# Kernel optimization log

Measured on AMD Instinct MI355X. Metric: run time of the kernel, lower is better.

Reference implementation:

```python
import jax, jax.numpy as jnp
import numpy as np

ENERGY = 0.4  # target low-frequency energy ratio (ctor default energy=0.4)


def setup_inputs() -> dict:
    key = jax.random.key(0)
    x = jax.random.normal(key, (8, 64, 256, 256), dtype=jnp.float32)
    return {"x": x}


def _min_cutoff_map(H, W):
    """For each pixel of the fftshifted spectrum, the smallest cutoff c such that
    the pixel lies inside the central box [crow-c:crow+c, ccol-c:ccol+c].
    A pixel (r, cc) is inside iff c >= max(-dr, dr+1) and c >= max(-dc, dc+1)."""
    crow, ccol = H // 2, W // 2
    dr = np.arange(H) - crow
    dc = np.arange(W) - ccol
    mr = np.maximum(-dr, dr + 1)
    mc = np.maximum(-dc, dc + 1)
    return np.maximum(mr[:, None], mc[None, :]).astype(np.int32)  # [H, W]


def reference(x):
    B, C, H, W = x.shape
    # fp32 FFT (matches the autocast-disabled fft in the original)
    fshift = jnp.fft.fftshift(jnp.fft.fft2(x.astype(jnp.float32)), axes=(-2, -1))

    minc = jnp.asarray(_min_cutoff_map(H, W))          # [H, W] int32
    nseg = max(H // 2, W // 2) + 1                      # static
    K = min(H, W) // 2                                  # candidates are 1..K-1

    # Radial (box) cumulative energy profile of channel 0, one pass per sample.
    mag2 = jnp.abs(fshift[:, 0]) ** 2                   # [B, H, W]
    ids = minc.reshape(-1)
    per_box = jax.vmap(
        lambda m: jax.ops.segment_sum(m.reshape(-1), ids, num_segments=nseg)
    )(mag2)                                             # [B, nseg]
    cum = jnp.cumsum(per_box, axis=-1)                  # cum[b, c] = box-energy at cutoff c
    total = cum[:, -1]
    target = ENERGY * total

    found = cum[:, 1:K] >= target[:, None]              # candidates c = 1..K-1
    first = jnp.argmax(found, axis=-1) + 1              # smallest satisfying c
    cutoff = jnp.where(jnp.any(found, axis=-1), first, 5)  # fallback 5, as in torch

    # Zero the central box per sample (broadcast over channels), then inverse FFT.
    keep = (minc[None, None, :, :] > cutoff[:, None, None, None]).astype(jnp.float32)
    hp = fshift * keep
    out = jnp.abs(jnp.fft.ifft2(jnp.fft.ifftshift(hp, axes=(-2, -1))))
    return out
```

## Files before the change

kernel.cpp:

```cpp
#include <hip/hip_runtime.h>
#include <hip/hip_fp16.h>
#include <math.h>

#define RESERVE 16384

__device__ __forceinline__ float2 cadd(float2 a, float2 b){ return make_float2(a.x+b.x, a.y+b.y); }
__device__ __forceinline__ float2 csub(float2 a, float2 b){ return make_float2(a.x-b.x, a.y-b.y); }
__device__ __forceinline__ float2 cmul(float2 a, float2 b){ return make_float2(a.x*b.x - a.y*b.y, a.x*b.y + a.y*b.x); }
__device__ __forceinline__ float2 cmulc(float2 a, float2 b){
  return make_float2(a.x*b.x + a.y*b.y, a.x*b.y - a.y*b.x); }
__device__ __forceinline__ __half2 f2h(float2 v){ return __floats2half2_rn(v.x, v.y); }
__device__ __forceinline__ float2 h2f(__half2 h){ return __half22float2(h); }

#define SCHED_FENCE() __builtin_amdgcn_sched_barrier(0x7F)

__device__ __forceinline__ constexpr int rho4(int r) { return ((r & 3) << 2) | (r >> 2); }

template<int DIR> __device__ __forceinline__ float2 twc(float2 z, float c, float s) {
  const float si = (DIR < 0) ? s : -s;
  return make_float2(c*z.x - si*z.y, c*z.y + si*z.x);
}
template<int DIR> __device__ __forceinline__ float2 mulmi(float2 z) {
  return (DIR < 0) ? make_float2(z.y, -z.x) : make_float2(-z.y, z.x);
}

template<int DIR, bool REV>
__device__ __forceinline__ void fft16(float2* v) {
  #define IX(i) (REV ? rho4(i) : (i))
  #pragma unroll
  for (int j0 = 0; j0 < 4; ++j0) {
    float2 a0 = v[IX(j0)], a1 = v[IX(j0+4)], a2 = v[IX(j0+8)], a3 = v[IX(j0+12)];
    float2 t0 = cadd(a0,a2), t1 = csub(a0,a2), t2 = cadd(a1,a3), d = csub(a1,a3);
    float2 t3 = (DIR < 0) ? make_float2(d.y,-d.x) : make_float2(-d.y,d.x);
    v[IX(j0)]    = cadd(t0,t2);
    v[IX(j0+4)]  = cadd(t1,t3);
    v[IX(j0+8)]  = csub(t0,t2);
    v[IX(j0+12)] = csub(t1,t3);
  }
  v[IX(5)]  = twc<DIR>(v[IX(5)],  0.92387953f, -0.38268343f);
  v[IX(6)]  = twc<DIR>(v[IX(6)],  0.70710678f, -0.70710678f);
  v[IX(7)]  = twc<DIR>(v[IX(7)],  0.38268343f, -0.92387953f);
  v[IX(9)]  = twc<DIR>(v[IX(9)],  0.70710678f, -0.70710678f);
  v[IX(10)] = mulmi<DIR>(v[IX(10)]);
  v[IX(11)] = twc<DIR>(v[IX(11)], -0.70710678f, -0.70710678f);
  v[IX(13)] = twc<DIR>(v[IX(13)],  0.38268343f, -0.92387953f);
  v[IX(14)] = twc<DIR>(v[IX(14)], -0.70710678f, -0.70710678f);
  v[IX(15)] = twc<DIR>(v[IX(15)], -0.92387953f,  0.38268343f);
  #pragma unroll
  for (int k1 = 0; k1 < 4; ++k1) {
    float2 a0 = v[IX(4*k1)], a1 = v[IX(4*k1+1)], a2 = v[IX(4*k1+2)], a3 = v[IX(4*k1+3)];
    float2 t0 = cadd(a0,a2), t1 = csub(a0,a2), t2 = cadd(a1,a3), d = csub(a1,a3);
    float2 t3 = (DIR < 0) ? make_float2(d.y,-d.x) : make_float2(-d.y,d.x);
    v[IX(4*k1)]   = cadd(t0,t2);
    v[IX(4*k1+1)] = cadd(t1,t3);
    v[IX(4*k1+2)] = csub(t0,t2);
    v[IX(4*k1+3)] = csub(t1,t3);
  }
  #undef IX
}

__device__ __forceinline__ void make_twf(int l, float2* twf) {
  float s, c;
  sincospif((float)l * (-1.0f/128.0f), &s, &c);
  const float2 w = make_float2(c, s);
  twf[0] = make_float2(1.f, 0.f);
  #pragma unroll
  for (int k = 1; k < 16; ++k) twf[k] = cmul(twf[k-1], w);
}

template<int DIR, bool REV1, bool HB>
__device__ __forceinline__ void fft256g(float2* v, void* trb, int l, const float2* twf) {
  fft16<DIR, REV1>(v);
  if (HB) {
    __half2* t = (__half2*)trb;
    #pragma unroll
    for (int r = 0; r < 16; ++r) {
      const int k1 = REV1 ? r : rho4(r);
      float2 z = v[r];
      z = (DIR < 0) ? cmul(twf[k1], z) : cmulc(twf[k1], z);
      t[k1 * 17 + l] = f2h(z);
    }
    SCHED_FENCE();
    #pragma unroll
    for (int j = 0; j < 16; ++j) v[j] = h2f(t[l * 17 + j]);
  } else {
    float2* t = (float2*)trb;
    #pragma unroll
    for (int r = 0; r < 16; ++r) {
      const int k1 = REV1 ? r : rho4(r);
      float2 z = v[r];
      z = (DIR < 0) ? cmul(twf[k1], z) : cmulc(twf[k1], z);
      t[k1 * 17 + l] = z;
    }
    SCHED_FENCE();
    #pragma unroll
    for (int j = 0; j < 16; ++j) v[j] = ((float2*)trb)[l * 17 + j];
  }
  SCHED_FENCE();
  fft16<DIR, false>(v);
}

#define GS32 276
#define GS16 280

__device__ __forceinline__ int SW(int row, int col) {
  return (row << 8) + (col ^ ((row & 7) << 2) ^ ((row & 1) << 4));
}
__device__ __forceinline__ int SW16(int r, int ul) {
  return (r << 4) + (ul ^ (r & 14));
}


__global__ __launch_bounds__(256) void k_pass1(const float* __restrict__ x,
    __half2* __restrict__ Bt, int img0, int istep) {
  __shared__ __align__(16) char smraw[16384];
  __shared__ __align__(16) float2 trbf[16 * GS32];
  float*   rowstage = (float*)smraw;
  __half2* outtile  = (__half2*)smraw;
  const int tid = threadIdx.x, g = tid >> 4, l = tid & 15;
  const int slot = blockIdx.y, img = img0 + slot * istep;
  const int r0 = blockIdx.x << 4;
  float2 twf[16]; make_twf(l, twf);
  const float* xsrc = x + ((size_t)img << 16) + (r0 << 8);
  #pragma unroll
  for (int it = 0; it < 4; ++it) {
    const int L = it * 1024 + tid * 4;
    const float4 d = *reinterpret_cast<const float4*>(xsrc + L);
    *reinterpret_cast<float4*>(rowstage + SW(L >> 8, L & 255)) = d;
  }
  __syncthreads();
  float2 v[16];
  #pragma unroll
  for (int j = 0; j < 16; ++j)
    v[j] = make_float2(rowstage[SW(g, l + (j << 4))], 0.f);
  __syncthreads();
  fft256g<-1, false, false>(v, trbf + g * GS32, l, twf);
  #pragma unroll
  for (int rr = 0; rr < 16; ++rr)
    outtile[SW(g, l + (rho4(rr) << 4))] = f2h(v[rr]);
  __syncthreads();
  __half2* bdst = Bt + ((size_t)slot << 16) + (r0 << 4);
  #pragma unroll
  for (int it = 0; it < 4; ++it) {
    const int L = it * 1024 + tid * 4;
    const int p = L >> 8, rl = (L >> 4) & 15, ul0 = L & 15;
    const int4 d = *reinterpret_cast<const int4*>(outtile + SW(rl, (p << 4) + ul0));
    *reinterpret_cast<int4*>(bdst + (p << 12) + (L & 255)) = d;
  }
}

__global__ __launch_bounds__(256) void k_pass2(const __half2* __restrict__ Bt,
    __half2* __restrict__ Ct, const int* __restrict__ cutoffs, int img0, int istep) {
  __shared__ __align__(16) char smraw[16384];
  __shared__ __align__(16) __half2 trbh[16 * GS16];
  __half2* instage = (__half2*)smraw;
  __half2* outtile = (__half2*)smraw;
  const int tid = threadIdx.x, g = tid >> 4, l = tid & 15;
  const int slot = blockIdx.y, img = img0 + slot * istep;
  const int p = blockIdx.x;
  const int cut = cutoffs[img >> 6];
  float2 twf[16]; make_twf(l, twf);
  const __half2* bsrc = Bt + ((size_t)slot << 16) + (p << 12);
  #pragma unroll
  for (int it = 0; it < 4; ++it) {
    const int L = it * 1024 + tid * 4;
    const int4 d = *reinterpret_cast<const int4*>(bsrc + L);
    const int r = L >> 4, ul0 = L & 15;
    const int i0 = SW16(r, ul0);
    *reinterpret_cast<int2*>(instage + i0) = make_int2(d.x, d.y);
    *reinterpret_cast<int2*>(instage + (i0 ^ 2)) = make_int2(d.z, d.w);
  }
  __syncthreads();
  __half2 hv[16];
  #pragma unroll
  for (int j = 0; j < 16; ++j) hv[j] = instage[SW16(l + (j << 4), g)];
  __syncthreads();
  const int u = (p << 4) + g;
  float2 v[16];
  #pragma unroll
  for (int j = 0; j < 16; ++j) v[j] = h2f(hv[j]);
  fft256g<-1, false, true>(v, trbh + g * GS16, l, twf);
  if ((u < cut) | (u >= 256 - cut)) {
    #pragma unroll
    for (int rr = 0; rr < 16; ++rr) {
      const int vi = l + (rho4(rr) << 4);
      if (vi < cut || vi >= 256 - cut) v[rr] = make_float2(0.f, 0.f);
    }
  }
  fft256g<1, true, true>(v, trbh + g * GS16, l, twf);
  #pragma unroll
  for (int rr = 0; rr < 16; ++rr)
    outtile[SW16(l + (rho4(rr) << 4), g)] = f2h(v[rr]);
  __syncthreads();
  __half2* cdst = Ct + ((size_t)slot << 16) + (p << 12);
  #pragma unroll
  for (int it = 0; it < 4; ++it) {
    const int L = it * 1024 + tid * 4;
    const int r = L >> 4, ul0 = L & 15;
    const int i0 = SW16(r, ul0);
    const int2 a = *reinterpret_cast<const int2*>(outtile + i0);
    const int2 b = *reinterpret_cast<const int2*>(outtile + (i0 ^ 2));
    *reinterpret_cast<int4*>(cdst + L) = make_int4(a.x, a.y, b.x, b.y);
  }
}

__global__ __launch_bounds__(256) void k_pass3(const __half2* __restrict__ Ct,
    float* __restrict__ out, int img0, int istep) {
  __shared__ __align__(16) char smraw[16384];
  __shared__ __align__(16) __half2 trbh[16 * GS16];
  __half2* instage  = (__half2*)smraw;
  float*   outstage = (float*)smraw;
  const int tid = threadIdx.x, g = tid >> 4, l = tid & 15;
  const int slot = blockIdx.y, img = img0 + slot * istep;
  const int r0 = blockIdx.x << 4;
  float2 twf[16]; make_twf(l, twf);
  #pragma unroll
  for (int k = 0; k < 16; ++k) { twf[k].x *= 0.0625f; twf[k].y *= 0.0625f; }
  const __half2* csrc = Ct + ((size_t)slot << 16) + (r0 << 4);
  #pragma unroll
  for (int it = 0; it < 4; ++it) {
    const int L = it * 1024 + tid * 4;
    const int p = L >> 8, rl = (L >> 4) & 15, ul0 = L & 15;
    const int4 d = *reinterpret_cast<const int4*>(csrc + (p << 12) + (L & 255));
    *reinterpret_cast<int4*>(instage + SW(rl, (p << 4) + ul0)) = d;
  }
  __syncthreads();
  __half2 hv[16];
  #pragma unroll
  for (int j = 0; j < 16; ++j) hv[j] = instage[SW(g, l + (j << 4))];
  __syncthreads();
  float2 v[16];
  #pragma unroll
  for (int j = 0; j < 16; ++j) v[j] = h2f(hv[j]);
  fft256g<1, false, true>(v, trbh + g * GS16, l, twf);
  #pragma unroll
  for (int rr = 0; rr < 16; ++rr) {
    const float2 z = v[rr];
    outstage[SW(g, l + (rho4(rr) << 4))] =
        __builtin_amdgcn_sqrtf(z.x*z.x + z.y*z.y) * (1.f/4096.f);
  }
  __syncthreads();
  float* odst = out + ((size_t)img << 16) + (r0 << 8);
  #pragma unroll
  for (int it = 0; it < 4; ++it) {
    const int L = it * 1024 + tid * 4;
    const float4 d = *reinterpret_cast<const float4*>(outstage + SW(L >> 8, L & 255));
    *reinterpret_cast<float4*>(odst + L) = d;
  }
}

__global__ __launch_bounds__(256) void k_hist(const __half2* __restrict__ Bt,
    double* __restrict__ bins, int slot0, int sstep, int batch0) {
  __shared__ __align__(16) __half2 instage[4096];
  __shared__ __align__(16) float2 trbf[16 * GS32];
  __shared__ float whist[4][132];
  const int tid = threadIdx.x, g = tid >> 4, l = tid & 15, wave = tid >> 6;
  const int lb = blockIdx.y;
  const int batch = batch0 + lb;
  const size_t slot = (size_t)(slot0 + lb * sstep);
  const int p = blockIdx.x;
  const int u = (p << 4) + g;
  float2 twf[16]; make_twf(l, twf);
  for (int i = tid & 63; i < 132; i += 64) whist[wave][i] = 0.f;
  const __half2* bsrc = Bt + (slot << 16) + (p << 12);
  #pragma unroll
  for (int it = 0; it < 4; ++it) {
    const int L = it * 1024 + tid * 4;
    const int4 d = *reinterpret_cast<const int4*>(bsrc + L);
    const int r = L >> 4, ul0 = L & 15;
    const int i0 = SW16(r, ul0);
    *reinterpret_cast<int2*>(instage + i0) = make_int2(d.x, d.y);
    *reinterpret_cast<int2*>(instage + (i0 ^ 2)) = make_int2(d.z, d.w);
  }
  __syncthreads();
  float2 v[16];
  #pragma unroll
  for (int j = 0; j < 16; ++j) v[j] = h2f(instage[SW16(l + (j << 4), g)]);
  fft256g<-1, false, false>(v, trbf + g * GS32, l, twf);
  const int fc = (u < 128) ? u + 1 : 256 - u;
  #pragma unroll
  for (int rr = 0; rr < 16; ++rr) {
    const int vi = l + (rho4(rr) << 4);
    const int fu = (vi < 128) ? vi + 1 : 256 - vi;
    const int seg = fu > fc ? fu : fc;
    const float2 z = v[rr];
    atomicAdd(&whist[wave][seg], z.x*z.x + z.y*z.y);
  }
  __syncthreads();
  for (int s = tid; s < 129; s += 256) {
    const float sum = whist[0][s] + whist[1][s] + whist[2][s] + whist[3][s];
    if (sum != 0.f) atomicAdd(&bins[batch * 129 + s], (double)sum);
  }
}

__global__ void k_cutoff(const double* __restrict__ bins, int* __restrict__ cutoffs) {
  const int b = threadIdx.x;
  if (b < 8) {
    const double* Bv = bins + b * 129;
    double total = 0.0;
    for (int s = 0; s < 129; ++s) total += Bv[s];
    const double target = 0.4 * total;
    double cum = Bv[0];
    int cut = 5;
    bool found = false;
    for (int s = 1; s <= 127; ++s) {
      cum += Bv[s];
      if (!found && cum >= target) { cut = s; found = true; }
    }
    cutoffs[b] = cut;
  }
}

extern "C" void kernel_launch(void* const* d_in, const int* in_sizes, int n_in,
                              void* d_out, int out_size, void* d_ws, size_t ws_size,
                              hipStream_t stream) {
  const float* x = (const float*)d_in[0];
  float* out = (float*)d_out;
  char* wsb = (char*)d_ws;
  double* bins    = (double*)wsb;
  int*    cutoffs = (int*)(wsb + 8448);
  char*   payload = wsb + RESERVE;

  size_t avail = (ws_size > RESERVE) ? ws_size - (size_t)RESERVE : 0;
  long long Gl = (long long)(avail / 524288);
  int G = (Gl > 512) ? 512 : (int)Gl;
  if (G < 1) G = 1;
  __half2* Bt = (__half2*)payload;
  __half2* Ct = (__half2*)(payload + (size_t)G * 262144);

  hipMemsetAsync(bins, 0, 8 * 129 * sizeof(double), stream);
  dim3 blk(256, 1, 1);

  if (G >= 512) {
    k_pass1<<<dim3(16, 512), blk, 0, stream>>>(x, Bt, 0, 1);
    k_hist <<<dim3(16, 8),   blk, 0, stream>>>(Bt, bins, 0, 64, 0);
    k_cutoff<<<dim3(1), dim3(64), 0, stream>>>(bins, cutoffs);
    k_pass2<<<dim3(16, 512), blk, 0, stream>>>(Bt, Ct, cutoffs, 0, 1);
    k_pass3<<<dim3(16, 512), blk, 0, stream>>>(Ct, out, 0, 1);
  } else {
    int Gp = G > 8 ? 8 : G;
    for (int b0 = 0; b0 < 8; b0 += Gp) {
      int n = (8 - b0 < Gp) ? (8 - b0) : Gp;
      k_pass1<<<dim3(16, n), blk, 0, stream>>>(x, Bt, b0 * 64, 64);
      k_hist <<<dim3(16, n), blk, 0, stream>>>(Bt, bins, 0, 1, b0);
    }
    k_cutoff<<<dim3(1), dim3(64), 0, stream>>>(bins, cutoffs);
    for (int g0 = 0; g0 < 512; g0 += G) {
      int n = (512 - g0 < G) ? (512 - g0) : G;
      k_pass1<<<dim3(16, n), blk, 0, stream>>>(x, Bt, g0, 1);
      k_pass2<<<dim3(16, n), blk, 0, stream>>>(Bt, Ct, cutoffs, g0, 1);
      k_pass3<<<dim3(16, n), blk, 0, stream>>>(Ct, out, g0, 1);
    }
  }
}
```

Baseline: 209.8 us.

## Skip identity column FFTs outside cutoff band and alias shared buffers

Pass2 blocks whose column group lies entirely outside the zeroed low-frequency band now exit early, because the forward and inverse column FFT would be an identity. Pass3 reads those columns directly from the row-FFT buffer, scaled by 256 to undo the missing normalization. Shared staging and transpose buffers are merged into one aliased region, with extra barriers, to reduce LDS use and allow more resident blocks. The fp16 rescale could lose precision or overflow, and how much work is skipped depends on the data-dependent cutoff.

```diff
diff --git a/kernel.cpp b/kernel.cpp
--- a/kernel.cpp
+++ b/kernel.cpp
@@ -113,10 +113,10 @@
 
 __global__ __launch_bounds__(256) void k_pass1(const float* __restrict__ x,
     __half2* __restrict__ Bt, int img0, int istep) {
-  __shared__ __align__(16) char smraw[16384];
-  __shared__ __align__(16) float2 trbf[16 * GS32];
+  __shared__ __align__(16) char smraw[16 * GS32 * 8];
   float*   rowstage = (float*)smraw;
   __half2* outtile  = (__half2*)smraw;
+  float2*  trbf     = (float2*)smraw;
   const int tid = threadIdx.x, g = tid >> 4, l = tid & 15;
   const int slot = blockIdx.y, img = img0 + slot * istep;
   const int r0 = blockIdx.x << 4;
@@ -135,6 +135,7 @@
     v[j] = make_float2(rowstage[SW(g, l + (j << 4))], 0.f);
   __syncthreads();
   fft256g<-1, false, false>(v, trbf + g * GS32, l, twf);
+  __syncthreads();
   #pragma unroll
   for (int rr = 0; rr < 16; ++rr)
     outtile[SW(g, l + (rho4(rr) << 4))] = f2h(v[rr]);
@@ -151,16 +152,19 @@
 
 __global__ __launch_bounds__(256) void k_pass2(const __half2* __restrict__ Bt,
     __half2* __restrict__ Ct, const int* __restrict__ cutoffs, int img0, int istep) {
-  __shared__ __align__(16) char smraw[16384];
-  __shared__ __align__(16) __half2 trbh[16 * GS16];
+  __shared__ __align__(16) char smraw[16 * GS16 * 4];
   __half2* instage = (__half2*)smraw;
   __half2* outtile = (__half2*)smraw;
+  __half2* trbh    = (__half2*)smraw;
   const int tid = threadIdx.x, g = tid >> 4, l = tid & 15;
   const int slot = blockIdx.y, img = img0 + slot * istep;
   const int p = blockIdx.x;
   const int cut = cutoffs[img >> 6];
+  const bool kept = (p * 16 >= cut) && (p * 16 + 15 < 256 - cut);
+  if (kept) return;
+  const __half2* bsrc = Bt + ((size_t)slot << 16) + (p << 12);
+  __half2* cdst = Ct + ((size_t)slot << 16) + (p << 12);
   float2 twf[16]; make_twf(l, twf);
-  const __half2* bsrc = Bt + ((size_t)slot << 16) + (p << 12);
   #pragma unroll
   for (int it = 0; it < 4; ++it) {
     const int L = it * 1024 + tid * 4;
@@ -188,11 +192,11 @@
     }
   }
   fft256g<1, true, true>(v, trbh + g * GS16, l, twf);
+  __syncthreads();
   #pragma unroll
   for (int rr = 0; rr < 16; ++rr)
     outtile[SW16(l + (rho4(rr) << 4), g)] = f2h(v[rr]);
   __syncthreads();
-  __half2* cdst = Ct + ((size_t)slot << 16) + (p << 12);
   #pragma unroll
   for (int it = 0; it < 4; ++it) {
     const int L = it * 1024 + tid * 4;
@@ -205,23 +209,34 @@
 }
 
 __global__ __launch_bounds__(256) void k_pass3(const __half2* __restrict__ Ct,
+    const __half2* __restrict__ Bt, const int* __restrict__ cutoffs,
     float* __restrict__ out, int img0, int istep) {
-  __shared__ __align__(16) char smraw[16384];
-  __shared__ __align__(16) __half2 trbh[16 * GS16];
+  __shared__ __align__(16) char smraw[16 * GS16 * 4];
   __half2* instage  = (__half2*)smraw;
   float*   outstage = (float*)smraw;
+  __half2* trbh     = (__half2*)smraw;
   const int tid = threadIdx.x, g = tid >> 4, l = tid & 15;
   const int slot = blockIdx.y, img = img0 + slot * istep;
   const int r0 = blockIdx.x << 4;
+  const int cut = cutoffs[img >> 6];
   float2 twf[16]; make_twf(l, twf);
   #pragma unroll
   for (int k = 0; k < 16; ++k) { twf[k].x *= 0.0625f; twf[k].y *= 0.0625f; }
   const __half2* csrc = Ct + ((size_t)slot << 16) + (r0 << 4);
+  const __half2* bsrc = Bt + ((size_t)slot << 16) + (r0 << 4);
+  const __half2 s256 = __floats2half2_rn(256.f, 256.f);
   #pragma unroll
   for (int it = 0; it < 4; ++it) {
     const int L = it * 1024 + tid * 4;
     const int p = L >> 8, rl = (L >> 4) & 15, ul0 = L & 15;
-    const int4 d = *reinterpret_cast<const int4*>(csrc + (p << 12) + (L & 255));
+    const bool kp = (p * 16 >= cut) && (p * 16 + 15 < 256 - cut);
+    const __half2* src = kp ? bsrc : csrc;
+    int4 d = *reinterpret_cast<const int4*>(src + (p << 12) + (L & 255));
+    if (kp) {
+      __half2* h = reinterpret_cast<__half2*>(&d);
+      h[0] = __hmul2(h[0], s256); h[1] = __hmul2(h[1], s256);
+      h[2] = __hmul2(h[2], s256); h[3] = __hmul2(h[3], s256);
+    }
     *reinterpret_cast<int4*>(instage + SW(rl, (p << 4) + ul0)) = d;
   }
   __syncthreads();
@@ -233,6 +248,7 @@
   #pragma unroll
   for (int j = 0; j < 16; ++j) v[j] = h2f(hv[j]);
   fft256g<1, false, true>(v, trbh + g * GS16, l, twf);
+  __syncthreads();
   #pragma unroll
   for (int rr = 0; rr < 16; ++rr) {
     const float2 z = v[rr];
@@ -336,7 +352,7 @@
     k_hist <<<dim3(16, 8),   blk, 0, stream>>>(Bt, bins, 0, 64, 0);
     k_cutoff<<<dim3(1), dim3(64), 0, stream>>>(bins, cutoffs);
     k_pass2<<<dim3(16, 512), blk, 0, stream>>>(Bt, Ct, cutoffs, 0, 1);
-    k_pass3<<<dim3(16, 512), blk, 0, stream>>>(Ct, out, 0, 1);
+    k_pass3<<<dim3(16, 512), blk, 0, stream>>>(Ct, Bt, cutoffs, out, 0, 1);
   } else {
     int Gp = G > 8 ? 8 : G;
     for (int b0 = 0; b0 < 8; b0 += Gp) {
@@ -349,7 +365,7 @@
       int n = (512 - g0 < G) ? (512 - g0) : G;
       k_pass1<<<dim3(16, n), blk, 0, stream>>>(x, Bt, g0, 1);
       k_pass2<<<dim3(16, n), blk, 0, stream>>>(Bt, Ct, cutoffs, g0, 1);
-      k_pass3<<<dim3(16, n), blk, 0, stream>>>(Ct, out, g0, 1);
-    }
-  }
-}
+      k_pass3<<<dim3(16, n), blk, 0, stream>>>(Ct, Bt, cutoffs, out, g0, 1);
+    }
+  }
+}
```

After: 222.0 us. 5.8% more time.
